# Kernel optimization log

Hardware: AMD Instinct MI355X
Metric: run time of the kernel (lower is better)

The kernel has to match this reference:

```python
import jax, jax.numpy as jnp
import numpy as np

B, C, S = 32, 2048, 28   # batch, in_channels, spatial_size
M, Q = 4, 1              # number of RAEs, hidden units per RAE
LAMBDA = 1e-3            # ridge regularization for the ELM-style decoder solve
EPS = 1e-10              # lp_norm_layer eps


def setup_inputs() -> dict:
    key = jax.random.key(0)
    k1, k2 = jax.random.split(key)
    x = jax.random.normal(k1, (B, C, S, S), dtype=jnp.float32)
    # Random (seeded, untrained) encoder weights for the M randomized autoencoders.
    W = jax.random.normal(k2, (M, C, Q), dtype=jnp.float32)
    return {"x": x, "W": W}


def _pos_encoding(n, d, dtype):
    # Standard sinusoidal 1D positional encoding over the n=H*W pixel positions,
    # d = channel dim (RADAM adds it to the per-pixel feature vectors).
    pos = jnp.arange(n, dtype=dtype)[:, None]                 # (n, 1)
    i = jnp.arange(0, d, 2, dtype=dtype)                      # (d/2,)
    div = jnp.exp(-(i / d) * jnp.log(jnp.asarray(10000.0, dtype)))
    pe = jnp.zeros((n, d), dtype)
    pe = pe.at[:, 0::2].set(jnp.sin(pos * div))
    pe = pe.at[:, 1::2].set(jnp.cos(pos * div))
    return pe


def reference(x, W):
    # x: (B, C, H, W) feature maps; W: (M, C, Q) random encoder weights.
    b, c, h, w = x.shape
    n = h * w
    # lp_norm_layer: L2-normalize each channel's spatial map jointly over (H, W).
    norm = jnp.sqrt(jnp.sum(x * x, axis=(2, 3), keepdims=True))
    xn = x / jnp.maximum(norm, EPS)
    # Resize(spatial_size) is identity (input already at spatial_size); flatten.
    feats = xn.reshape(b, c, n).transpose(0, 2, 1)            # (B, N, C) pixels-as-samples
    pe = _pos_encoding(n, c, x.dtype)                         # (N, C)
    xp = feats + pe[None]                                     # pos-encoded input
    # Hidden activations of all M RAEs for all batch elements at once.
    hid = jax.nn.sigmoid(jnp.einsum('bnc,mcq->bmnq', xp, W))  # (B, M, N, Q)
    # Closed-form ridge (ELM) decoder: beta = (H^T H + lam I)^{-1} H^T X
    hth = jnp.einsum('bmnq,bmnp->bmqp', hid, hid)             # (B, M, Q, Q)
    htx = jnp.einsum('bmnq,bnc->bmqc', hid, xp)               # (B, M, Q, C)
    eye = LAMBDA * jnp.eye(Q, dtype=x.dtype)
    beta = jnp.linalg.solve(hth + eye, htx)                   # (B, M, Q, C)
    # Sum decoder weights over the M RAEs (the per-rae pooled += in the loop).
    pooled = jnp.nan_to_num(jnp.sum(beta, axis=1))            # (B, Q, C)
    return pooled
```

## Files before the change

kernel.cpp:

```cpp
#include <hip/hip_runtime.h>
#include <math.h>

#define BB 32
#define CC 2048
#define NN 784
#define NF4 196
#define MM 4
#define NCH 32
#define CPER (CC / NCH)
#define LAMBDA_ 1e-3f
#define EPS_ 1e-10f
#define LOG1E4 9.210340371976184f
#define NORMB (BB * CC / 4)
#define OUT_BLOCKS (BB * CC / 4)

__device__ __forceinline__ float wred(float v) {
#pragma unroll
  for (int off = 32; off > 0; off >>= 1) v += __shfl_down(v, off, 64);
  return v;
}

__global__ __launch_bounds__(256) void k_norm_w(const float* __restrict__ x,
                                                const float* __restrict__ W,
                                                float* __restrict__ inv_norm,
                                                float* __restrict__ Ws,
                                                float* __restrict__ peW) {
  int bid  = blockIdx.x;
  int wv   = threadIdx.x >> 6;
  int lane = threadIdx.x & 63;

  if (bid >= NORMB) {
    int n = bid - NORMB;
    int m = wv;
    float acc = 0.f;
    for (int c = lane; c < CC; c += 64) {
      float di  = __expf(-((float)(c & ~1) * (1.f / CC)) * LOG1E4);
      float arg = (float)n * di;
      float pe  = (c & 1) ? __cosf(arg) : __sinf(arg);
      acc += pe * W[m * CC + c];
    }
    acc = wred(acc);
    if (lane == 0) peW[m * NN + n] = acc;
    return;
  }

  int idx = bid * 4 + wv;
  int b = idx >> 11;
  int c = idx & (CC - 1);
  const float4* row = (const float4*)(x + (size_t)idx * NN);
  float4 v0 = row[lane];
  float4 v1 = row[lane + 64];
  float4 v2 = row[lane + 128];
  float4 v3 = (lane < (NF4 - 192)) ? row[lane + 192] : make_float4(0.f, 0.f, 0.f, 0.f);
  float ss = v0.x*v0.x + v0.y*v0.y + v0.z*v0.z + v0.w*v0.w
           + v1.x*v1.x + v1.y*v1.y + v1.z*v1.z + v1.w*v1.w
           + v2.x*v2.x + v2.y*v2.y + v2.z*v2.z + v2.w*v2.w
           + v3.x*v3.x + v3.y*v3.y + v3.z*v3.z + v3.w*v3.w;
  ss = wred(ss);
  if (lane == 0) {
    float inv = 1.f / fmaxf(sqrtf(ss), EPS_);
    inv_norm[idx] = inv;
#pragma unroll
    for (int m = 0; m < MM; ++m)
      Ws[((size_t)b * MM + m) * CC + c] = W[m * CC + c] * inv;
  }
}

__global__ __launch_bounds__(256) void k_sacc3(const float* __restrict__ x,
                                               const float* __restrict__ Ws,
                                               float4* __restrict__ sPart4) {
  int t  = threadIdx.x;
  int ch = blockIdx.x;
  int b  = blockIdx.y;
  if (t >= NF4) return;
  int c0 = ch * CPER;
  const float4* xb = (const float4*)(x + ((size_t)b * CC + c0) * NN) + t;
  const float* wb  = Ws + (size_t)b * MM * CC + c0;

  float4 a0{0,0,0,0}, a1{0,0,0,0}, a2{0,0,0,0}, a3{0,0,0,0};

  for (int i = 0; i < CPER; i += 8) {
    float4 xv[8];
#pragma unroll
    for (int u = 0; u < 8; ++u) xv[u] = xb[(size_t)(i + u) * NF4];
#pragma unroll
    for (int u = 0; u < 8; ++u) {
      int c = i + u;
      float w0 = wb[0 * CC + c];
      float w1 = wb[1 * CC + c];
      float w2 = wb[2 * CC + c];
      float w3 = wb[3 * CC + c];
      float4 v = xv[u];
      a0.x += v.x * w0; a0.y += v.y * w0; a0.z += v.z * w0; a0.w += v.w * w0;
      a1.x += v.x * w1; a1.y += v.y * w1; a1.z += v.z * w1; a1.w += v.w * w1;
      a2.x += v.x * w2; a2.y += v.y * w2; a2.z += v.z * w2; a2.w += v.w * w2;
      a3.x += v.x * w3; a3.y += v.y * w3; a3.z += v.z * w3; a3.w += v.w * w3;
    }
  }
  size_t base = (((size_t)b * NCH + ch) * MM) * NF4 + t;
  sPart4[base + 0 * NF4] = a0;
  sPart4[base + 1 * NF4] = a1;
  sPart4[base + 2 * NF4] = a2;
  sPart4[base + 3 * NF4] = a3;
}

__global__ __launch_bounds__(256) void k_hid(const float* __restrict__ sPart,
                                             const float* __restrict__ peW,
                                             float* __restrict__ hid4) {
  int n = blockIdx.x * 256 + threadIdx.x;
  int b = blockIdx.y;
  if (n >= NN) return;
  float h[MM];
#pragma unroll
  for (int m = 0; m < MM; ++m) {
    float s = peW[m * NN + n];
#pragma unroll 8
    for (int ch = 0; ch < NCH; ++ch)
      s += sPart[(((size_t)b * NCH + ch) * MM + m) * NN + n];
    h[m] = 1.f / (1.f + __expf(-s));
  }
  float4 hv = make_float4(h[0], h[1], h[2], h[3]);
  *(float4*)(hid4 + ((size_t)b * NN + n) * 4) = hv;
}

__global__ __launch_bounds__(256) void k_out(const float* __restrict__ x,
                                             const float* __restrict__ hid4,
                                             const float* __restrict__ inv_norm,
                                             float* __restrict__ out) {
  int idx  = blockIdx.x * 4 + (threadIdx.x >> 6);
  int lane = threadIdx.x & 63;
  int b = idx >> 11;
  int c = idx & (CC - 1);
  const float4* row = (const float4*)(x + (size_t)idx * NN);
  const float4* hb  = (const float4*)(hid4 + (size_t)b * NN * 4);
  float di = __expf(-((float)(c & ~1) * (1.0f / CC)) * LOG1E4);
  bool use_sin = !(c & 1);
  float aX0=0,aX1=0,aX2=0,aX3=0, aP0=0,aP1=0,aP2=0,aP3=0, aD0=0,aD1=0,aD2=0,aD3=0;
  for (int f = lane; f < NF4; f += 64) {
    float4 xv = row[f];
    int n = f * 4;
    float4 h0 = hb[n + 0], h1 = hb[n + 1], h2 = hb[n + 2], h3 = hb[n + 3];
    float a0 = (float)(n + 0) * di, a1 = (float)(n + 1) * di;
    float a2 = (float)(n + 2) * di, a3 = (float)(n + 3) * di;
    float p0 = use_sin ? __sinf(a0) : __cosf(a0);
    float p1 = use_sin ? __sinf(a1) : __cosf(a1);
    float p2 = use_sin ? __sinf(a2) : __cosf(a2);
    float p3 = use_sin ? __sinf(a3) : __cosf(a3);
    aX0 += xv.x*h0.x + xv.y*h1.x + xv.z*h2.x + xv.w*h3.x;
    aX1 += xv.x*h0.y + xv.y*h1.y + xv.z*h2.y + xv.w*h3.y;
    aX2 += xv.x*h0.z + xv.y*h1.z + xv.z*h2.z + xv.w*h3.z;
    aX3 += xv.x*h0.w + xv.y*h1.w + xv.z*h2.w + xv.w*h3.w;
    aP0 += p0*h0.x + p1*h1.x + p2*h2.x + p3*h3.x;
    aP1 += p0*h0.y + p1*h1.y + p2*h2.y + p3*h3.y;
    aP2 += p0*h0.z + p1*h1.z + p2*h2.z + p3*h3.z;
    aP3 += p0*h0.w + p1*h1.w + p2*h2.w + p3*h3.w;
    aD0 += h0.x*h0.x + h1.x*h1.x + h2.x*h2.x + h3.x*h3.x;
    aD1 += h0.y*h0.y + h1.y*h1.y + h2.y*h2.y + h3.y*h3.y;
    aD2 += h0.z*h0.z + h1.z*h1.z + h2.z*h2.z + h3.z*h3.z;
    aD3 += h0.w*h0.w + h1.w*h1.w + h2.w*h2.w + h3.w*h3.w;
  }
  aX0 = wred(aX0); aX1 = wred(aX1); aX2 = wred(aX2); aX3 = wred(aX3);
  aP0 = wred(aP0); aP1 = wred(aP1); aP2 = wred(aP2); aP3 = wred(aP3);
  aD0 = wred(aD0); aD1 = wred(aD1); aD2 = wred(aD2); aD3 = wred(aD3);
  if (lane == 0) {
    float inv = inv_norm[idx];
    float r = (inv * aX0 + aP0) / (aD0 + LAMBDA_)
            + (inv * aX1 + aP1) / (aD1 + LAMBDA_)
            + (inv * aX2 + aP2) / (aD2 + LAMBDA_)
            + (inv * aX3 + aP3) / (aD3 + LAMBDA_);
    if (isnan(r)) r = 0.f;
    else if (isinf(r)) r = (r > 0.f) ? 3.4028234663852886e38f : -3.4028234663852886e38f;
    out[idx] = r;
  }
}

extern "C" void kernel_launch(void* const* d_in, const int* in_sizes, int n_in,
                              void* d_out, int out_size, void* d_ws, size_t ws_size,
                              hipStream_t stream) {
  const float* x = (const float*)d_in[0];
  const float* W = (const float*)d_in[1];
  float* out = (float*)d_out;
  float* ws  = (float*)d_ws;

  float* inv_norm = ws;
  float* peW      = inv_norm + (size_t)BB * CC;
  float* hid4     = peW + (size_t)MM * NN;
  float* Ws       = hid4 + (size_t)BB * NN * MM;
  float* sPart    = Ws + (size_t)BB * MM * CC;

  k_norm_w<<<NORMB + NN, 256, 0, stream>>>(x, W, inv_norm, Ws, peW);
  k_sacc3<<<dim3(NCH, BB), 256, 0, stream>>>(x, Ws, (float4*)sPart);
  k_hid<<<dim3(4, BB), 256, 0, stream>>>(sPart, peW, hid4);
  k_out<<<OUT_BLOCKS, 256, 0, stream>>>(x, hid4, inv_norm, out);
}
```

Baseline: 144.7 us.

## Stage weights in LDS, hoist H^T H into hid kernel, use sincos recurrence

```diff
diff --git a/kernel.cpp b/kernel.cpp
--- a/kernel.cpp
+++ b/kernel.cpp
@@ -6,7 +6,7 @@
 #define NN 784
 #define NF4 196
 #define MM 4
-#define NCH 32
+#define NCH 64
 #define CPER (CC / NCH)
 #define LAMBDA_ 1e-3f
 #define EPS_ 1e-10f
@@ -66,17 +66,23 @@
   }
 }
 
-__global__ __launch_bounds__(256) void k_sacc3(const float* __restrict__ x,
+__global__ __launch_bounds__(256) void k_sacc4(const float* __restrict__ x,
                                                const float* __restrict__ Ws,
                                                float4* __restrict__ sPart4) {
   int t  = threadIdx.x;
   int ch = blockIdx.x;
   int b  = blockIdx.y;
+  int c0 = ch * CPER;
+
+  __shared__ float wlds[MM][CPER];
+  if (t < MM * CPER) {
+    int m = t >> 5, i = t & (CPER - 1);
+    wlds[m][i] = Ws[((size_t)b * MM + m) * CC + c0 + i];
+  }
+  __syncthreads();
   if (t >= NF4) return;
-  int c0 = ch * CPER;
+
   const float4* xb = (const float4*)(x + ((size_t)b * CC + c0) * NN) + t;
-  const float* wb  = Ws + (size_t)b * MM * CC + c0;
-
   float4 a0{0,0,0,0}, a1{0,0,0,0}, a2{0,0,0,0}, a3{0,0,0,0};
 
   for (int i = 0; i < CPER; i += 8) {
@@ -85,11 +91,10 @@
     for (int u = 0; u < 8; ++u) xv[u] = xb[(size_t)(i + u) * NF4];
 #pragma unroll
     for (int u = 0; u < 8; ++u) {
-      int c = i + u;
-      float w0 = wb[0 * CC + c];
-      float w1 = wb[1 * CC + c];
-      float w2 = wb[2 * CC + c];
-      float w3 = wb[3 * CC + c];
+      float w0 = wlds[0][i + u];
+      float w1 = wlds[1][i + u];
+      float w2 = wlds[2][i + u];
+      float w3 = wlds[3][i + u];
       float4 v = xv[u];
       a0.x += v.x * w0; a0.y += v.y * w0; a0.z += v.z * w0; a0.w += v.w * w0;
       a1.x += v.x * w1; a1.y += v.y * w1; a1.z += v.z * w1; a1.w += v.w * w1;
@@ -104,29 +109,51 @@
   sPart4[base + 3 * NF4] = a3;
 }
 
-__global__ __launch_bounds__(256) void k_hid(const float* __restrict__ sPart,
-                                             const float* __restrict__ peW,
-                                             float* __restrict__ hid4) {
-  int n = blockIdx.x * 256 + threadIdx.x;
+__global__ __launch_bounds__(256) void k_hid2(const float* __restrict__ sPart,
+                                              const float* __restrict__ peW,
+                                              float* __restrict__ hid4,
+                                              float* __restrict__ aDpart) {
+  int g = blockIdx.x;
   int b = blockIdx.y;
-  if (n >= NN) return;
+  int t = threadIdx.x;
+  int n = g * 256 + t;
+  bool valid = n < NN;
+  int wv = t >> 6, lane = t & 63;
+
   float h[MM];
 #pragma unroll
   for (int m = 0; m < MM; ++m) {
-    float s = peW[m * NN + n];
+    float hm = 0.f;
+    if (valid) {
+      float s = peW[m * NN + n];
 #pragma unroll 8
-    for (int ch = 0; ch < NCH; ++ch)
-      s += sPart[(((size_t)b * NCH + ch) * MM + m) * NN + n];
-    h[m] = 1.f / (1.f + __expf(-s));
-  }
-  float4 hv = make_float4(h[0], h[1], h[2], h[3]);
-  *(float4*)(hid4 + ((size_t)b * NN + n) * 4) = hv;
-}
-
-__global__ __launch_bounds__(256) void k_out(const float* __restrict__ x,
-                                             const float* __restrict__ hid4,
-                                             const float* __restrict__ inv_norm,
-                                             float* __restrict__ out) {
+      for (int ch = 0; ch < NCH; ++ch)
+        s += sPart[(((size_t)b * NCH + ch) * MM + m) * NN + n];
+      hm = 1.f / (1.f + __expf(-s));
+    }
+    h[m] = hm;
+  }
+  if (valid) {
+    float4 hv = make_float4(h[0], h[1], h[2], h[3]);
+    *(float4*)(hid4 + ((size_t)b * NN + n) * 4) = hv;
+  }
+
+  __shared__ float red[4][MM];
+#pragma unroll
+  for (int m = 0; m < MM; ++m) {
+    float q = wred(h[m] * h[m]);
+    if (lane == 0) red[wv][m] = q;
+  }
+  __syncthreads();
+  if (t < MM)
+    aDpart[((size_t)b * 4 + g) * MM + t] = red[0][t] + red[1][t] + red[2][t] + red[3][t];
+}
+
+__global__ __launch_bounds__(256) void k_out2(const float* __restrict__ x,
+                                              const float* __restrict__ hid4,
+                                              const float* __restrict__ inv_norm,
+                                              const float* __restrict__ aDpart,
+                                              float* __restrict__ out) {
   int idx  = blockIdx.x * 4 + (threadIdx.x >> 6);
   int lane = threadIdx.x & 63;
   int b = idx >> 11;
@@ -135,17 +162,30 @@
   const float4* hb  = (const float4*)(hid4 + (size_t)b * NN * 4);
   float di = __expf(-((float)(c & ~1) * (1.0f / CC)) * LOG1E4);
   bool use_sin = !(c & 1);
-  float aX0=0,aX1=0,aX2=0,aX3=0, aP0=0,aP1=0,aP2=0,aP3=0, aD0=0,aD1=0,aD2=0,aD3=0;
+
+  float s, cO;  __sincosf((float)(4 * lane) * di, &s, &cO);
+  float s1, c1; __sincosf(di, &s1, &c1);
+  float s2 = 2.f * s1 * c1, c2 = 1.f - 2.f * s1 * s1;
+  float s3 = s1 * c2 + c1 * s2, c3 = c1 * c2 - s1 * s2;
+  float SD, CD; __sincosf(256.f * di, &SD, &CD);
+
+  float aX0=0,aX1=0,aX2=0,aX3=0, aP0=0,aP1=0,aP2=0,aP3=0;
   for (int f = lane; f < NF4; f += 64) {
     float4 xv = row[f];
     int n = f * 4;
     float4 h0 = hb[n + 0], h1 = hb[n + 1], h2 = hb[n + 2], h3 = hb[n + 3];
-    float a0 = (float)(n + 0) * di, a1 = (float)(n + 1) * di;
-    float a2 = (float)(n + 2) * di, a3 = (float)(n + 3) * di;
-    float p0 = use_sin ? __sinf(a0) : __cosf(a0);
-    float p1 = use_sin ? __sinf(a1) : __cosf(a1);
-    float p2 = use_sin ? __sinf(a2) : __cosf(a2);
-    float p3 = use_sin ? __sinf(a3) : __cosf(a3);
+    float p0, p1, p2, p3;
+    if (use_sin) {
+      p0 = s;
+      p1 = s * c1 + cO * s1;
+      p2 = s * c2 + cO * s2;
+      p3 = s * c3 + cO * s3;
+    } else {
+      p0 = cO;
+      p1 = cO * c1 - s * s1;
+      p2 = cO * c2 - s * s2;
+      p3 = cO * c3 - s * s3;
+    }
     aX0 += xv.x*h0.x + xv.y*h1.x + xv.z*h2.x + xv.w*h3.x;
     aX1 += xv.x*h0.y + xv.y*h1.y + xv.z*h2.y + xv.w*h3.y;
     aX2 += xv.x*h0.z + xv.y*h1.z + xv.z*h2.z + xv.w*h3.z;
@@ -154,15 +194,18 @@
     aP1 += p0*h0.y + p1*h1.y + p2*h2.y + p3*h3.y;
     aP2 += p0*h0.z + p1*h1.z + p2*h2.z + p3*h3.z;
     aP3 += p0*h0.w + p1*h1.w + p2*h2.w + p3*h3.w;
-    aD0 += h0.x*h0.x + h1.x*h1.x + h2.x*h2.x + h3.x*h3.x;
-    aD1 += h0.y*h0.y + h1.y*h1.y + h2.y*h2.y + h3.y*h3.y;
-    aD2 += h0.z*h0.z + h1.z*h1.z + h2.z*h2.z + h3.z*h3.z;
-    aD3 += h0.w*h0.w + h1.w*h1.w + h2.w*h2.w + h3.w*h3.w;
+    float ns = s * CD + cO * SD;
+    float nc = cO * CD - s * SD;
+    s = ns; cO = nc;
   }
   aX0 = wred(aX0); aX1 = wred(aX1); aX2 = wred(aX2); aX3 = wred(aX3);
   aP0 = wred(aP0); aP1 = wred(aP1); aP2 = wred(aP2); aP3 = wred(aP3);
-  aD0 = wred(aD0); aD1 = wred(aD1); aD2 = wred(aD2); aD3 = wred(aD3);
   if (lane == 0) {
+    const float* ad = aDpart + (size_t)b * 4 * MM;
+    float aD0 = ad[0] + ad[4] + ad[8]  + ad[12];
+    float aD1 = ad[1] + ad[5] + ad[9]  + ad[13];
+    float aD2 = ad[2] + ad[6] + ad[10] + ad[14];
+    float aD3 = ad[3] + ad[7] + ad[11] + ad[15];
     float inv = inv_norm[idx];
     float r = (inv * aX0 + aP0) / (aD0 + LAMBDA_)
             + (inv * aX1 + aP1) / (aD1 + LAMBDA_)
@@ -186,10 +229,11 @@
   float* peW      = inv_norm + (size_t)BB * CC;
   float* hid4     = peW + (size_t)MM * NN;
   float* Ws       = hid4 + (size_t)BB * NN * MM;
-  float* sPart    = Ws + (size_t)BB * MM * CC;
+  float* aDpart   = Ws + (size_t)BB * MM * CC;
+  float* sPart    = aDpart + (size_t)BB * 4 * MM;
 
   k_norm_w<<<NORMB + NN, 256, 0, stream>>>(x, W, inv_norm, Ws, peW);
-  k_sacc3<<<dim3(NCH, BB), 256, 0, stream>>>(x, Ws, (float4*)sPart);
-  k_hid<<<dim3(4, BB), 256, 0, stream>>>(sPart, peW, hid4);
-  k_out<<<OUT_BLOCKS, 256, 0, stream>>>(x, hid4, inv_norm, out);
-}
+  k_sacc4<<<dim3(NCH, BB), 256, 0, stream>>>(x, Ws, (float4*)sPart);
+  k_hid2<<<dim3(4, BB), 256, 0, stream>>>(sPart, peW, hid4, aDpart);
+  k_out2<<<OUT_BLOCKS, 256, 0, stream>>>(x, hid4, inv_norm, aDpart, out);
+}
```

Measured after the change: 160.8 us. +11.1%, slower.
